# Kernel tuning notes

Hardware: AMD Instinct MI355X
Metric: run time of the kernel (lower is better)

## Reference

```python
import jax, jax.numpy as jnp
import numpy as np

NUM_HEADS = 8
SCALE = 25.0
SIM_THRESH = 0.75


def setup_inputs() -> dict:
    key = jax.random.key(0)
    k1, k2, k3, k4 = jax.random.split(key, 4)
    B, N, C = 1, 2048, 1024
    x_cls = jax.random.normal(k1, (B, N, C), jnp.float32)
    cls_score = jax.random.uniform(k2, (N,), jnp.float32)
    fg_score = jax.random.uniform(k3, (N,), jnp.float32)
    W_qkv = jax.random.normal(k4, (3 * C, C), jnp.float32) * 0.02
    return {"x_cls": x_cls, "cls_score": cls_score, "fg_score": fg_score, "W_qkv": W_qkv}


def reference(x_cls, cls_score, fg_score, W_qkv):
    B, N, C = x_cls.shape
    H = NUM_HEADS
    hd = C // H
    # qkv projection (Linear without bias): [B,N,3C] -> [3,B,H,N,hd]
    qkv = (x_cls @ W_qkv.T).reshape(B, N, 3, H, hd).transpose(2, 0, 3, 1, 4)
    q, k, v = qkv[0], qkv[1], qkv[2]
    # cosine normalization
    qn = q / jnp.linalg.norm(q, axis=-1, keepdims=True)
    kn = k / jnp.linalg.norm(k, axis=-1, keepdims=True)
    vn = v / jnp.linalg.norm(v, axis=-1, keepdims=True)
    # cls_score broadcast to [1,1,1,N] (columns); fg_score is unused downstream
    cs = cls_score.reshape(1, 1, 1, N)
    # raw v-v similarity map [B,H,N,N]
    attn_cls_raw = vn @ jnp.swapaxes(vn, -2, -1)
    # use_mask=True path: mask[i,j] = cls_score[j] > cls_score[i] - 0.1
    cs_mask = (cs > jnp.swapaxes(cs, -2, -1) - 0.1).astype(x_cls.dtype)
    # scaled, score-weighted, masked attention; dropout p=0 is identity
    attn = jax.nn.softmax((qn @ jnp.swapaxes(kn, -2, -1)) * SCALE * cs * cs_mask, axis=-1)
    x = jnp.swapaxes(attn @ v, 1, 2).reshape(B, N, C)
    x_ori = jnp.swapaxes(v, 1, 2).reshape(B, N, C)
    x_out = jnp.concatenate([x, x_ori], axis=-1)  # [B,N,2C]
    # ave=True branch: head-averaged similarity + second softmax, masked renorm
    sim_raw = attn_cls_raw.sum(axis=1)[0] / H  # [N,N]
    sim_mask = (sim_raw > SIM_THRESH).astype(x_cls.dtype)
    sim_attn = attn.sum(axis=1)[0] / H
    sim_round2 = jax.nn.softmax(sim_attn, axis=-1)
    masked = sim_mask * sim_round2
    sim_round2 = masked / jnp.sum(masked, axis=-1, keepdims=True)
    return (x_out, sim_round2)
```

## Files before the change

### kernel.cpp

```cpp
#include <hip/hip_runtime.h>
#include <cstdint>

typedef unsigned short u16;
typedef __attribute__((ext_vector_type(8))) short short8;
typedef __attribute__((ext_vector_type(4))) short short4v;
typedef __attribute__((ext_vector_type(4))) float f32x4;

#define NTOK 2048
#define CDIM 1024
#define C3   3072
#define NH   8
#define HD   128

__device__ __forceinline__ float bf2f(u16 u) {
    return __uint_as_float(((unsigned)u) << 16);
}
__device__ __forceinline__ u16 f2bf(float f) {
    unsigned u = __float_as_uint(f);
    u += 0x7fffu + ((u >> 16) & 1u);
    return (u16)(u >> 16);
}
__device__ __forceinline__ void gld_lds16(const u16* g, u16* l) {
    __builtin_amdgcn_global_load_lds(
        (__attribute__((address_space(1))) void*)(u16*)g,
        (__attribute__((address_space(3))) void*)l, 16, 0, 0);
}

__global__ __launch_bounds__(256) void k_cast(const float* __restrict__ x,
                                              const float* __restrict__ w,
                                              u16* __restrict__ xb,
                                              u16* __restrict__ wb) {
    int t = blockIdx.x * blockDim.x + threadIdx.x;
    int stride = gridDim.x * blockDim.x;
    for (int i = t; i < (NTOK * CDIM) / 4; i += stride) {
        float4 v = ((const float4*)x)[i];
        ushort4 o;
        o.x = f2bf(v.x); o.y = f2bf(v.y); o.z = f2bf(v.z); o.w = f2bf(v.w);
        ((ushort4*)xb)[i] = o;
    }
    for (int i = t; i < (C3 * CDIM) / 4; i += stride) {
        float4 v = ((const float4*)w)[i];
        ushort4 o;
        o.x = f2bf(v.x); o.y = f2bf(v.y); o.z = f2bf(v.z); o.w = f2bf(v.w);
        ((ushort4*)wb)[i] = o;
    }
}

template <int EPI>
__global__ __launch_bounds__(256) void k_gemm64(const u16* __restrict__ A,
                                                const u16* __restrict__ B,
                                                void* __restrict__ Cv, int K,
                                                int lda, int ldb, int ldc,
                                                float scale) {
    if (EPI == 2 && blockIdx.x > blockIdx.y) return;
    __shared__ u16 As[128 * 64];
    __shared__ u16 Bs[128 * 64];
    const int tid = threadIdx.x;
    const int lane = tid & 63;
    const int wid = tid >> 6;
    const int wm = wid >> 1, wn = wid & 1;
    const int q = lane >> 4, l16 = lane & 15;
    const int m0 = blockIdx.y * 128, n0 = blockIdx.x * 128;

    f32x4 zero4 = {0.f, 0.f, 0.f, 0.f};
    f32x4 acc[4][4];
#pragma unroll
    for (int i = 0; i < 4; i++)
#pragma unroll
        for (int j = 0; j < 4; j++) acc[i][j] = zero4;

    const u16* aP[4];
    const u16* bP[4];
#pragma unroll
    for (int t = 0; t < 4; t++) {
        int s = tid + t * 256;
        int r = s >> 3, c = (s & 7) * 8;
        aP[t] = &A[(long long)(m0 + r) * lda + c];
        bP[t] = &B[(long long)(n0 + r) * ldb + c];
    }

    for (int k0 = 0; k0 < K; k0 += 64) {
        __syncthreads();
#pragma unroll
        for (int t = 0; t < 4; t++) {
            int s = tid + t * 256;
            gld_lds16(aP[t] + k0, &As[s * 8]);
            gld_lds16(bP[t] + k0, &Bs[s * 8]);
        }
        __syncthreads();
#pragma unroll
        for (int ks = 0; ks < 2; ks++) {
            short8 af[4], bfr[4];
#pragma unroll
            for (int tm = 0; tm < 4; tm++)
                af[tm] = *(const short8*)&As[(wm * 64 + tm * 16 + l16) * 64 + ks * 32 + q * 8];
#pragma unroll
            for (int tn = 0; tn < 4; tn++)
                bfr[tn] = *(const short8*)&Bs[(wn * 64 + tn * 16 + l16) * 64 + ks * 32 + q * 8];
#pragma unroll
            for (int tm = 0; tm < 4; tm++)
#pragma unroll
                for (int tn = 0; tn < 4; tn++)
                    acc[tm][tn] = __builtin_amdgcn_mfma_f32_16x16x32_bf16(
                        af[tm], bfr[tn], acc[tm][tn], 0, 0, 0);
        }
    }

#pragma unroll
    for (int tm = 0; tm < 4; tm++)
#pragma unroll
        for (int tn = 0; tn < 4; tn++)
#pragma unroll
            for (int r = 0; r < 4; r++) {
                int row = m0 + wm * 64 + tm * 16 + q * 4 + r;
                int col = n0 + wn * 64 + tn * 16 + l16;
                float v = acc[tm][tn][r];
                if (EPI == 0) {
                    ((u16*)Cv)[(long long)row * ldc + col] = f2bf(v);
                } else {
                    unsigned char b = (v * scale > 0.75f) ? 1 : 0;
                    ((unsigned char*)Cv)[(long long)row * ldc + col] = b;
                    ((unsigned char*)Cv)[(long long)col * ldc + row] = b;
                }
            }
}

__global__ __launch_bounds__(256) void k_norm(const u16* __restrict__ qkv,
                                              u16* __restrict__ Qn,
                                              u16* __restrict__ Kn,
                                              u16* __restrict__ Vn,
                                              float* __restrict__ out) {
    const int n = blockIdx.x;
    const int t = threadIdx.x;
    const int g16 = t >> 4;
    const int l16 = t & 15;
    const int d0 = l16 * 8;
#pragma unroll
    for (int s = 0; s < 2; s++) {
        int row = s * 16 + g16;
        if (row < 24) {
            int which = row >> 3;
            int h = row & 7;
            const u16* src = qkv + (long long)n * C3 + which * CDIM + h * HD + d0;
            short8 v8 = *(const short8*)src;
            float f[8];
            float ss = 0.f;
#pragma unroll
            for (int k = 0; k < 8; k++) {
                f[k] = bf2f((u16)v8[k]);
                ss += f[k] * f[k];
            }
            ss += __shfl_xor(ss, 1);
            ss += __shfl_xor(ss, 2);
            ss += __shfl_xor(ss, 4);
            ss += __shfl_xor(ss, 8);
            float rn = rsqrtf(ss);
            u16* dst = (which == 0 ? Qn : which == 1 ? Kn : Vn) +
                       (long long)n * CDIM + h * HD + d0;
            short8 o8;
#pragma unroll
            for (int k = 0; k < 8; k++) o8[k] = (short)f2bf(f[k] * rn);
            *(short8*)dst = o8;
            if (which == 2) {
                float4 a, b;
                a.x = f[0]; a.y = f[1]; a.z = f[2]; a.w = f[3];
                b.x = f[4]; b.y = f[5]; b.z = f[6]; b.w = f[7];
                float* od = &out[(long long)n * 2048 + 1024 + h * HD + d0];
                *(float4*)od = a;
                *(float4*)(od + 4) = b;
            }
        }
    }
}

__global__ __launch_bounds__(256) void k_vt(const u16* __restrict__ qkv,
                                            u16* __restrict__ Vt) {
    __shared__ u16 T[64][72];
    const int n0 = blockIdx.x * 64;
    const int c0 = blockIdx.y * 64;
    const int tid = threadIdx.x;
    {
        int nl = tid >> 2, cc = (tid & 3) * 16;
        const u16* src = &qkv[(long long)(n0 + nl) * C3 + 2 * CDIM + c0 + cc];
        *(short8*)&T[nl][cc] = *(const short8*)&src[0];
        *(short8*)&T[nl][cc + 8] = *(const short8*)&src[8];
    }
    __syncthreads();
    {
        int cl = tid >> 2, nc = (tid & 3) * 16;
        ushort va[16];
#pragma unroll
        for (int i = 0; i < 16; i++) va[i] = T[nc + i][cl];
        u16* dst = &Vt[(long long)(c0 + cl) * NTOK + n0 + nc];
        *(short8*)&dst[0] = *(short8*)&va[0];
        *(short8*)&dst[8] = *(short8*)&va[8];
    }
}

__global__ __launch_bounds__(256, 4) void k_attn7(const u16* __restrict__ Qn,
                                                  const u16* __restrict__ Kn,
                                                  const u16* __restrict__ Vt,
                                                  const float* __restrict__ cls,
                                                  u16* __restrict__ P,
                                                  float* __restrict__ Spart,
                                                  u16* __restrict__ Xpart) {
    __shared__ u16 Kf[16384];
    __shared__ u16 Vf[16384];
    __shared__ u16 Et[4096];
    const int h = blockIdx.z;
    const int jc = blockIdx.y;
    const int i0 = blockIdx.x * 64;
    const int jbase = jc * 512;
    const int tid = threadIdx.x, lane = tid & 63, wid = tid >> 6;
    const int q = lane >> 4, l16 = lane & 15;
    const int wm = wid >> 1, wn = wid & 1;

    short8 af[2][4];
#pragma unroll
    for (int m = 0; m < 2; m++)
#pragma unroll
        for (int kt = 0; kt < 4; kt++)
            af[m][kt] = *(const short8*)&Qn[(long long)(i0 + wm * 32 + m * 16 + l16) * CDIM +
                                            h * HD + kt * 32 + q * 8];
    float cls_i[2][4];
#pragma unroll
    for (int m = 0; m < 2; m++)
#pragma unroll
        for (int r = 0; r < 4; r++)
            cls_i[m][r] = cls[i0 + wm * 32 + m * 16 + q * 4 + r] - 0.1f;

    const u16* ksrc[4];
    const u16* vsrc[4];
#pragma unroll
    for (int t = 0; t < 4; t++) {
        int g = wid * 4 + t;
        int tn = g >> 2, kt = g & 3;
        ksrc[t] = &Kn[(long long)(jbase + tn * 16 + l16) * CDIM + h * HD + kt * 32 + q * 8];
        int n = g >> 1, ks = g & 1;
        vsrc[t] = &Vt[(long long)(h * HD + n * 16 + l16) * NTOK + jbase + (ks * 4 + q) * 8];
    }

    f32x4 zero4 = {0.f, 0.f, 0.f, 0.f};
    f32x4 pv[2][4];
#pragma unroll
    for (int m = 0; m < 2; m++)
#pragma unroll
        for (int n = 0; n < 4; n++) pv[m][n] = zero4;
    float sums[2][4] = {{0.f, 0.f, 0.f, 0.f}, {0.f, 0.f, 0.f, 0.f}};

    for (int jt = 0; jt < 8; ++jt) {
        const int j0 = jbase + jt * 64;
        __syncthreads();
#pragma unroll
        for (int t = 0; t < 4; t++) {
            int g = wid * 4 + t;
            gld_lds16(ksrc[t], &Kf[(g * 64 + lane) * 8]);
            gld_lds16(vsrc[t], &Vf[(g * 64 + lane) * 8]);
            ksrc[t] += 64 * CDIM;
            vsrc[t] += 64;
        }
        __syncthreads();
#pragma unroll
        for (int tn = 0; tn < 2; tn++) {
            int tng = wn * 2 + tn;
            short8 bfr[4];
#pragma unroll
            for (int kt = 0; kt < 4; kt++)
                bfr[kt] = *(const short8*)&Kf[((tng * 4 + kt) * 64 + lane) * 8];
            int j = j0 + tng * 16 + l16;
            float cj = cls[j];
            float sc = 25.f * cj;
#pragma unroll
            for (int m = 0; m < 2; m++) {
                f32x4 acc = zero4;
#pragma unroll
                for (int kt = 0; kt < 4; kt++)
                    acc = __builtin_amdgcn_mfma_f32_16x16x32_bf16(af[m][kt], bfr[kt],
                                                                  acc, 0, 0, 0);
                int ibase = wm * 32 + m * 16 + q * 4;
#pragma unroll
                for (int r = 0; r < 4; r++) {
                    float mk = (cj > cls_i[m][r]) ? 1.f : 0.f;
                    float e = __expf(acc[r] * sc * mk);
                    sums[m][r] += e;
                    int il = ibase + r;
                    int jl = tng * 16 + l16;
                    Et[il * 64 + ((((jl >> 3) ^ (il & 7)) << 3) | (jl & 7))] = f2bf(e);
                }
            }
        }
        __syncthreads();
        {
            int il = tid >> 2, c = tid & 3;
            int x = il & 7;
            short8 e0 = *(const short8*)&Et[il * 64 + (((2 * c) ^ x) << 3)];
            short8 e1 = *(const short8*)&Et[il * 64 + (((2 * c + 1) ^ x) << 3)];
            u16* dst = &P[((long long)(h * NTOK + i0 + il)) * NTOK + j0 + c * 16];
            *(short8*)&dst[0] = e0;
            *(short8*)&dst[8] = e1;
        }
#pragma unroll
        for (int ks = 0; ks < 2; ks++) {
            short8 a2[2];
#pragma unroll
            for (int m2 = 0; m2 < 2; m2++) {
                int il = wm * 32 + m2 * 16 + l16;
                int ch = ks * 4 + q;
                a2[m2] = *(const short8*)&Et[il * 64 + ((ch ^ (il & 7)) << 3)];
            }
#pragma unroll
            for (int n2 = 0; n2 < 4; n2++) {
                short8 b2 = *(const short8*)&Vf[(((wn * 4 + n2) * 2 + ks) * 64 + lane) * 8];
#pragma unroll
                for (int m2 = 0; m2 < 2; m2++)
                    pv[m2][n2] = __builtin_amdgcn_mfma_f32_16x16x32_bf16(
                        a2[m2], b2, pv[m2][n2], 0, 0, 0);
            }
        }
    }
#pragma unroll
    for (int m = 0; m < 2; m++)
#pragma unroll
        for (int r = 0; r < 4; r++) {
            float s = sums[m][r];
            s += __shfl_xor(s, 1);
            s += __shfl_xor(s, 2);
            s += __shfl_xor(s, 4);
            s += __shfl_xor(s, 8);
            if (l16 == 0)
                Spart[((wn * 4 + jc) * NH + h) * NTOK + i0 + wm * 32 + m * 16 + q * 4 + r] = s;
        }
    u16* Xp = Xpart + (long long)jc * NTOK * CDIM;
#pragma unroll
    for (int m2 = 0; m2 < 2; m2++)
#pragma unroll
        for (int n2 = 0; n2 < 4; n2++)
#pragma unroll
            for (int r = 0; r < 4; r++) {
                int i = i0 + wm * 32 + m2 * 16 + q * 4 + r;
                int d = wn * 64 + n2 * 16 + l16;
                Xp[(long long)i * CDIM + h * HD + d] = f2bf(pv[m2][n2][r]);
            }
}

__global__ __launch_bounds__(256) void k_epi(const u16* __restrict__ Xpart,
                                             const float* __restrict__ Spart,
                                             const u16* __restrict__ P,
                                             const unsigned char* __restrict__ mask,
                                             float* __restrict__ out,
                                             float* __restrict__ out2) {
    __shared__ float red[256];
    __shared__ float sArr[NH];
    const int i = blockIdx.x;
    const int t = threadIdx.x;
    if (t < NH) {
        float s = 0.f;
#pragma unroll
        for (int g = 0; g < 8; g++) s += Spart[(g * NH + t) * NTOK + i];
        sArr[t] = s;
    }
    __syncthreads();
    {
        int c = t * 4;
        int h = c >> 7;
        float acc[4] = {0.f, 0.f, 0.f, 0.f};
#pragma unroll
        for (int jc = 0; jc < 4; jc++) {
            short4v v = *(const short4v*)&Xpart[(long long)jc * NTOK * CDIM +
                                                (long long)i * CDIM + c];
#pragma unroll
            for (int k = 0; k < 4; k++) acc[k] += bf2f((u16)v[k]);
        }
        float invs = 1.f / sArr[h];
        float4 o;
        o.x = acc[0] * invs; o.y = acc[1] * invs; o.z = acc[2] * invs; o.w = acc[3] * invs;
        *(float4*)&out[(long long)i * 2048 + c] = o;
    }
    float invS[NH];
#pragma unroll
    for (int h = 0; h < NH; h++) invS[h] = 1.f / (8.f * sArr[h]);
    const int c0 = t * 8;
    float a[8] = {0.f, 0.f, 0.f, 0.f, 0.f, 0.f, 0.f, 0.f};
#pragma unroll
    for (int h = 0; h < NH; h++) {
        short8 p = *(const short8*)&P[((long long)h * NTOK + i) * NTOK + c0];
#pragma unroll
        for (int k = 0; k < 8; k++) a[k] += bf2f((u16)p[k]) * invS[h];
    }
    const unsigned char* mrow = mask + (long long)i * NTOK + c0;
    float e[8];
    unsigned char mk[8];
    float part = 0.f;
#pragma unroll
    for (int k = 0; k < 8; k++) {
        e[k] = __expf(a[k]);
        mk[k] = mrow[k];
        if (mk[k]) part += e[k];
    }
    red[t] = part;
    __syncthreads();
    for (int s = 128; s > 0; s >>= 1) {
        if (t < s) red[t] += red[t + s];
        __syncthreads();
    }
    float invT = 1.f / red[0];
    float o[8];
#pragma unroll
    for (int k = 0; k < 8; k++) o[k] = mk[k] ? e[k] * invT : 0.f;
    float4 o0, o1;
    o0.x = o[0]; o0.y = o[1]; o0.z = o[2]; o0.w = o[3];
    o1.x = o[4]; o1.y = o[5]; o1.z = o[6]; o1.w = o[7];
    float* dst = out2 + (long long)i * NTOK + c0;
    *(float4*)dst = o0;
    *(float4*)(dst + 4) = o1;
}

extern "C" void kernel_launch(void* const* d_in, const int* in_sizes, int n_in,
                              void* d_out, int out_size, void* d_ws,
                              size_t ws_size, hipStream_t stream) {
    (void)in_sizes; (void)n_in; (void)out_size; (void)ws_size;
    const float* x = (const float*)d_in[0];
    const float* cls = (const float*)d_in[1];
    const float* Wq = (const float*)d_in[3];
    float* out = (float*)d_out;
    char* ws = (char*)d_ws;

    u16* Xb = (u16*)(ws + 0);
    u16* Wb = (u16*)(ws + 4194304);
    u16* QKVb = (u16*)(ws + 10485760);
    u16* Xpart = (u16*)(ws + 0);
    float* Spart = (float*)(ws + 16777216);
    u16* Qn = (u16*)(ws + 23068672);
    u16* Kn = (u16*)(ws + 27262976);
    u16* Vn = (u16*)(ws + 31457280);
    u16* Vt = (u16*)(ws + 35651584);
    unsigned char* mask = (unsigned char*)(ws + 39845888);
    u16* P = (u16*)(ws + 44040192);

    k_cast<<<1024, 256, 0, stream>>>(x, Wq, Xb, Wb);

    k_gemm64<0><<<dim3(C3 / 128, NTOK / 128), 256, 0, stream>>>(
        Xb, Wb, QKVb, CDIM, CDIM, CDIM, C3, 1.f);

    k_norm<<<NTOK, 256, 0, stream>>>(QKVb, Qn, Kn, Vn, out);

    k_vt<<<dim3(NTOK / 64, CDIM / 64), 256, 0, stream>>>(QKVb, Vt);

    k_gemm64<2><<<dim3(16, 16), 256, 0, stream>>>(
        Vn, Vn, mask, CDIM, CDIM, CDIM, NTOK, 0.125f);

    k_attn7<<<dim3(32, 4, NH), 256, 0, stream>>>(Qn, Kn, Vt, cls, P, Spart, Xpart);

    k_epi<<<NTOK, 256, 0, stream>>>(Xpart, Spart, P, mask, out,
                                    out + (long long)NTOK * 2048);
}
```

Baseline: 223.5 us.

## Fuse QKV projection with per-head normalization and V transpose epilogue

Replaces the QKV GEMM, the normalization kernel and the V transpose kernel with a single GEMM whose 128-wide N tile matches one head. Row L2 norms are reduced in registers and LDS in the epilogue, normalized Q/K/V are written directly, and V blocks also write the fp32 x_ori output and a transposed V via LDS. This removes the intermediate bf16 QKV buffer round trip and two launches. In exchange the epilogue does scattered 2-byte stores and extra LDS syncs, and norms are now computed from fp32 accumulators rather than bf16-rounded values.

New measurement: 219.7 us. Within noise of the previous version (-1.7%).

```diff
diff --git a/kernel.cpp b/kernel.cpp
--- a/kernel.cpp
+++ b/kernel.cpp
@@ -46,13 +46,141 @@
     }
 }
 
-template <int EPI>
-__global__ __launch_bounds__(256) void k_gemm64(const u16* __restrict__ A,
-                                                const u16* __restrict__ B,
-                                                void* __restrict__ Cv, int K,
-                                                int lda, int ldb, int ldc,
-                                                float scale) {
-    if (EPI == 2 && blockIdx.x > blockIdx.y) return;
+__global__ __launch_bounds__(256) void k_qkvn(const u16* __restrict__ A,
+                                              const u16* __restrict__ B,
+                                              u16* __restrict__ Qn,
+                                              u16* __restrict__ Kn,
+                                              u16* __restrict__ Vn,
+                                              u16* __restrict__ Vt,
+                                              float* __restrict__ out) {
+    __shared__ u16 lds[128 * 136];
+    __shared__ float rowssq[128][2];
+    u16* As = lds;
+    u16* Bs = lds + 128 * 64;
+    const int tid = threadIdx.x;
+    const int lane = tid & 63;
+    const int wid = tid >> 6;
+    const int wm = wid >> 1, wn = wid & 1;
+    const int q = lane >> 4, l16 = lane & 15;
+    const int s = blockIdx.x;
+    const int which = s >> 3, h = s & 7;
+    const int m0 = blockIdx.y * 128, n0 = s * 128;
+
+    f32x4 zero4 = {0.f, 0.f, 0.f, 0.f};
+    f32x4 acc[4][4];
+#pragma unroll
+    for (int i = 0; i < 4; i++)
+#pragma unroll
+        for (int j = 0; j < 4; j++) acc[i][j] = zero4;
+
+    const u16* aP[4];
+    const u16* bP[4];
+#pragma unroll
+    for (int t = 0; t < 4; t++) {
+        int sl = tid + t * 256;
+        int r = sl >> 3, c = (sl & 7) * 8;
+        aP[t] = &A[(long long)(m0 + r) * CDIM + c];
+        bP[t] = &B[(long long)(n0 + r) * CDIM + c];
+    }
+
+    for (int k0 = 0; k0 < CDIM; k0 += 64) {
+        __syncthreads();
+#pragma unroll
+        for (int t = 0; t < 4; t++) {
+            int sl = tid + t * 256;
+            gld_lds16(aP[t] + k0, &As[sl * 8]);
+            gld_lds16(bP[t] + k0, &Bs[sl * 8]);
+        }
+        __syncthreads();
+#pragma unroll
+        for (int ks = 0; ks < 2; ks++) {
+            short8 af[4], bfr[4];
+#pragma unroll
+            for (int tm = 0; tm < 4; tm++)
+                af[tm] = *(const short8*)&As[(wm * 64 + tm * 16 + l16) * 64 + ks * 32 + q * 8];
+#pragma unroll
+            for (int tn = 0; tn < 4; tn++)
+                bfr[tn] = *(const short8*)&Bs[(wn * 64 + tn * 16 + l16) * 64 + ks * 32 + q * 8];
+#pragma unroll
+            for (int tm = 0; tm < 4; tm++)
+#pragma unroll
+                for (int tn = 0; tn < 4; tn++)
+                    acc[tm][tn] = __builtin_amdgcn_mfma_f32_16x16x32_bf16(
+                        af[tm], bfr[tn], acc[tm][tn], 0, 0, 0);
+        }
+    }
+
+    __syncthreads();
+#pragma unroll
+    for (int tm = 0; tm < 4; tm++)
+#pragma unroll
+        for (int r = 0; r < 4; r++) {
+            float p = 0.f;
+#pragma unroll
+            for (int tn = 0; tn < 4; tn++) p += acc[tm][tn][r] * acc[tm][tn][r];
+            p += __shfl_xor(p, 1);
+            p += __shfl_xor(p, 2);
+            p += __shfl_xor(p, 4);
+            p += __shfl_xor(p, 8);
+            if (l16 == 0) rowssq[wm * 64 + tm * 16 + q * 4 + r][wn] = p;
+        }
+    __syncthreads();
+    float rinv[4][4];
+#pragma unroll
+    for (int tm = 0; tm < 4; tm++)
+#pragma unroll
+        for (int r = 0; r < 4; r++) {
+            int rl = wm * 64 + tm * 16 + q * 4 + r;
+            rinv[tm][r] = rsqrtf(rowssq[rl][0] + rowssq[rl][1]);
+        }
+    u16* dstBase = (which == 0 ? Qn : which == 1 ? Kn : Vn);
+#pragma unroll
+    for (int tm = 0; tm < 4; tm++)
+#pragma unroll
+        for (int tn = 0; tn < 4; tn++)
+#pragma unroll
+            for (int r = 0; r < 4; r++) {
+                int rl = wm * 64 + tm * 16 + q * 4 + r;
+                int d = wn * 64 + tn * 16 + l16;
+                dstBase[(long long)(m0 + rl) * CDIM + h * HD + d] =
+                    f2bf(acc[tm][tn][r] * rinv[tm][r]);
+            }
+    if (which == 2) {
+#pragma unroll
+        for (int tm = 0; tm < 4; tm++)
+#pragma unroll
+            for (int tn = 0; tn < 4; tn++)
+#pragma unroll
+                for (int r = 0; r < 4; r++) {
+                    int rl = wm * 64 + tm * 16 + q * 4 + r;
+                    int d = wn * 64 + tn * 16 + l16;
+                    float v = acc[tm][tn][r];
+                    out[(long long)(m0 + rl) * 2048 + 1024 + h * HD + d] = v;
+                    lds[rl * 136 + d] = f2bf(v);
+                }
+        __syncthreads();
+#pragma unroll
+        for (int p = 0; p < 2; p++) {
+            int drow = p * 64 + (tid >> 2);
+            int nc = (tid & 3) * 32;
+            u16 buf[32];
+#pragma unroll
+            for (int i = 0; i < 32; i++) buf[i] = lds[(nc + i) * 136 + drow];
+            u16* dst = &Vt[(long long)(h * HD + drow) * NTOK + m0 + nc];
+            *(short8*)&dst[0] = *(short8*)&buf[0];
+            *(short8*)&dst[8] = *(short8*)&buf[8];
+            *(short8*)&dst[16] = *(short8*)&buf[16];
+            *(short8*)&dst[24] = *(short8*)&buf[24];
+        }
+    }
+}
+
+__global__ __launch_bounds__(256) void k_gemm_mask(const u16* __restrict__ A,
+                                                   const u16* __restrict__ B,
+                                                   unsigned char* __restrict__ Cv,
+                                                   int K, int lda, int ldb, int ldc,
+                                                   float scale) {
+    if (blockIdx.x > blockIdx.y) return;
     __shared__ u16 As[128 * 64];
     __shared__ u16 Bs[128 * 64];
     const int tid = threadIdx.x;
@@ -114,87 +242,10 @@
             for (int r = 0; r < 4; r++) {
                 int row = m0 + wm * 64 + tm * 16 + q * 4 + r;
                 int col = n0 + wn * 64 + tn * 16 + l16;
-                float v = acc[tm][tn][r];
-                if (EPI == 0) {
-                    ((u16*)Cv)[(long long)row * ldc + col] = f2bf(v);
-                } else {
-                    unsigned char b = (v * scale > 0.75f) ? 1 : 0;
-                    ((unsigned char*)Cv)[(long long)row * ldc + col] = b;
-                    ((unsigned char*)Cv)[(long long)col * ldc + row] = b;
-                }
+                unsigned char b = (acc[tm][tn][r] * scale > 0.75f) ? 1 : 0;
+                Cv[(long long)row * ldc + col] = b;
+                Cv[(long long)col * ldc + row] = b;
             }
-}
-
-__global__ __launch_bounds__(256) void k_norm(const u16* __restrict__ qkv,
-                                              u16* __restrict__ Qn,
-                                              u16* __restrict__ Kn,
-                                              u16* __restrict__ Vn,
-                                              float* __restrict__ out) {
-    const int n = blockIdx.x;
-    const int t = threadIdx.x;
-    const int g16 = t >> 4;
-    const int l16 = t & 15;
-    const int d0 = l16 * 8;
-#pragma unroll
-    for (int s = 0; s < 2; s++) {
-        int row = s * 16 + g16;
-        if (row < 24) {
-            int which = row >> 3;
-            int h = row & 7;
-            const u16* src = qkv + (long long)n * C3 + which * CDIM + h * HD + d0;
-            short8 v8 = *(const short8*)src;
-            float f[8];
-            float ss = 0.f;
-#pragma unroll
-            for (int k = 0; k < 8; k++) {
-                f[k] = bf2f((u16)v8[k]);
-                ss += f[k] * f[k];
-            }
-            ss += __shfl_xor(ss, 1);
-            ss += __shfl_xor(ss, 2);
-            ss += __shfl_xor(ss, 4);
-            ss += __shfl_xor(ss, 8);
-            float rn = rsqrtf(ss);
-            u16* dst = (which == 0 ? Qn : which == 1 ? Kn : Vn) +
-                       (long long)n * CDIM + h * HD + d0;
-            short8 o8;
-#pragma unroll
-            for (int k = 0; k < 8; k++) o8[k] = (short)f2bf(f[k] * rn);
-            *(short8*)dst = o8;
-            if (which == 2) {
-                float4 a, b;
-                a.x = f[0]; a.y = f[1]; a.z = f[2]; a.w = f[3];
-                b.x = f[4]; b.y = f[5]; b.z = f[6]; b.w = f[7];
-                float* od = &out[(long long)n * 2048 + 1024 + h * HD + d0];
-                *(float4*)od = a;
-                *(float4*)(od + 4) = b;
-            }
-        }
-    }
-}
-
-__global__ __launch_bounds__(256) void k_vt(const u16* __restrict__ qkv,
-                                            u16* __restrict__ Vt) {
-    __shared__ u16 T[64][72];
-    const int n0 = blockIdx.x * 64;
-    const int c0 = blockIdx.y * 64;
-    const int tid = threadIdx.x;
-    {
-        int nl = tid >> 2, cc = (tid & 3) * 16;
-        const u16* src = &qkv[(long long)(n0 + nl) * C3 + 2 * CDIM + c0 + cc];
-        *(short8*)&T[nl][cc] = *(const short8*)&src[0];
-        *(short8*)&T[nl][cc + 8] = *(const short8*)&src[8];
-    }
-    __syncthreads();
-    {
-        int cl = tid >> 2, nc = (tid & 3) * 16;
-        ushort va[16];
-#pragma unroll
-        for (int i = 0; i < 16; i++) va[i] = T[nc + i][cl];
-        u16* dst = &Vt[(long long)(c0 + cl) * NTOK + n0 + nc];
-        *(short8*)&dst[0] = *(short8*)&va[0];
-        *(short8*)&dst[8] = *(short8*)&va[8];
-    }
 }
 
 __global__ __launch_bounds__(256, 4) void k_attn7(const u16* __restrict__ Qn,
@@ -427,7 +478,6 @@
 
     u16* Xb = (u16*)(ws + 0);
     u16* Wb = (u16*)(ws + 4194304);
-    u16* QKVb = (u16*)(ws + 10485760);
     u16* Xpart = (u16*)(ws + 0);
     float* Spart = (float*)(ws + 16777216);
     u16* Qn = (u16*)(ws + 23068672);
@@ -439,14 +489,9 @@
 
     k_cast<<<1024, 256, 0, stream>>>(x, Wq, Xb, Wb);
 
-    k_gemm64<0><<<dim3(C3 / 128, NTOK / 128), 256, 0, stream>>>(
-        Xb, Wb, QKVb, CDIM, CDIM, CDIM, C3, 1.f);
-
-    k_norm<<<NTOK, 256, 0, stream>>>(QKVb, Qn, Kn, Vn, out);
-
-    k_vt<<<dim3(NTOK / 64, CDIM / 64), 256, 0, stream>>>(QKVb, Vt);
-
-    k_gemm64<2><<<dim3(16, 16), 256, 0, stream>>>(
+    k_qkvn<<<dim3(24, 16), 256, 0, stream>>>(Xb, Wb, Qn, Kn, Vn, Vt, out);
+
+    k_gemm_mask<<<dim3(16, 16), 256, 0, stream>>>(
         Vn, Vn, mask, CDIM, CDIM, CDIM, NTOK, 0.125f);
 
     k_attn7<<<dim3(32, 4, NH), 256, 0, stream>>>(Qn, Kn, Vt, cls, P, Spart, Xpart);
```
